# Optimization experiments

Measured on AMD Instinct MI355X. Metric: run time of the kernel, lower is better.

Reference implementation:

```python
import jax, jax.numpy as jnp
import numpy as np

B, S, D = 2, 2048, 2048
H, KV, HD = 32, 8, 64  # num_heads, num_key_value_heads, head_dim
ROPE_BASE = 10000.0


def setup_inputs() -> dict:
    key = jax.random.key(0)
    k1, k2, k3 = jax.random.split(key, 3)
    x = jax.random.normal(k1, (B, S, D), dtype=jnp.float32)
    # torch Linear weights are [out_features, in_features]
    w_qkv = jax.random.normal(k2, (H * HD + 2 * KV * HD, D), dtype=jnp.float32) * (D ** -0.5)
    w_out = jax.random.normal(k3, (D, D), dtype=jnp.float32) * (D ** -0.5)
    # true RoPE tables: cos/sin are [S, HD] with the half-frequencies duplicated
    inv_freq = 1.0 / (ROPE_BASE ** (jnp.arange(0, HD, 2, dtype=jnp.float32) / HD))
    angles = jnp.arange(S, dtype=jnp.float32)[:, None] * inv_freq[None, :]  # [S, HD/2]
    emb = jnp.concatenate([angles, angles], axis=-1)  # [S, HD]
    return {"x": x, "cos": jnp.cos(emb), "sin": jnp.sin(emb), "w_qkv": w_qkv, "w_out": w_out}


def _apply_rope(t, cos, sin):
    # t: [B, h, S, HD]; cos/sin: [S, HD]
    half = t.shape[-1] // 2
    t1, t2 = t[..., :half], t[..., half:]
    rot = jnp.concatenate([-t2, t1], axis=-1)
    return t * cos[None, None, :, :] + rot * sin[None, None, :, :]


def reference(x, cos, sin, w_qkv, w_out):
    b, s, d = x.shape
    qkv = jnp.einsum('bsd,od->bso', x, w_qkv)  # merged QKV projection
    q, k, v = jnp.split(qkv, [H * HD, H * HD + KV * HD], axis=-1)
    q = q.reshape(b, s, H, HD).transpose(0, 2, 1, 3)   # [b,H,s,hd]
    k = k.reshape(b, s, KV, HD).transpose(0, 2, 1, 3)  # [b,KV,s,hd]
    v = v.reshape(b, s, KV, HD).transpose(0, 2, 1, 3)
    q = _apply_rope(q, cos, sin)
    k = _apply_rope(k, cos, sin)
    n_rep = H // KV
    k = jnp.repeat(k, n_rep, axis=1)  # repeat_kv -> [b,H,s,hd]
    v = jnp.repeat(v, n_rep, axis=1)
    scale = HD ** -0.5
    scores = jnp.einsum('bhqd,bhkd->bhqk', q, k) * scale
    causal = jnp.tril(jnp.ones((s, s), dtype=bool))
    scores = jnp.where(causal[None, None], scores, jnp.finfo(scores.dtype).min)
    attn = jax.nn.softmax(scores, axis=-1)
    out = jnp.einsum('bhqk,bhkd->bhqd', attn, v)
    out = out.transpose(0, 2, 1, 3).reshape(b, s, H * HD)
    return jnp.einsum('bso,do->bsd', out, w_out)
```

## Files before the change

### kernel.cpp

```cpp
#include <hip/hip_runtime.h>
#include <hip/hip_fp16.h>

#define B_ 2
#define S_ 2048
#define D_ 2048
#define H_ 32
#define KV_ 8
#define HD_ 64

typedef unsigned short bf16_t;
typedef __attribute__((ext_vector_type(8))) short short8;
typedef __attribute__((ext_vector_type(4))) float floatx4;
typedef __attribute__((ext_vector_type(2))) float float2v;

__device__ __forceinline__ bf16_t f2bf(float f) {
  union { float f; unsigned u; } c; c.f = f;
  unsigned u = c.u;
  u += 0x7fffu + ((u >> 16) & 1u);
  return (bf16_t)(u >> 16);
}

__device__ __forceinline__ unsigned pk_bf16(float a, float b) {
#if __has_builtin(__builtin_amdgcn_cvt_pk_bf16_f32)
  auto v = __builtin_amdgcn_cvt_pk_bf16_f32(a, b);
  unsigned u; __builtin_memcpy(&u, &v, 4); return u;
#else
  return (unsigned)f2bf(a) | ((unsigned)f2bf(b) << 16);
#endif
}

__device__ __forceinline__ float fexp2(float x) {
#if __has_builtin(__builtin_amdgcn_exp2f)
  return __builtin_amdgcn_exp2f(x);
#else
  return exp2f(x);
#endif
}

__device__ __forceinline__ void load_lds16(const void* g, void* l) {
  __builtin_amdgcn_global_load_lds(
      (const __attribute__((address_space(1))) void*)g,
      (__attribute__((address_space(3))) void*)l, 16, 0, 0);
}

__device__ __forceinline__ void cvt4(const float* __restrict__ in,
                                     bf16_t* __restrict__ out, int i) {
  float4 v = ((const float4*)in)[i];
  ushort4 o;
  o.x = f2bf(v.x); o.y = f2bf(v.y); o.z = f2bf(v.z); o.w = f2bf(v.w);
  ((ushort4*)out)[i] = o;
}

__global__ __launch_bounds__(256) void prep(
    const float* __restrict__ x, bf16_t* __restrict__ xb,
    const float* __restrict__ wqkv, bf16_t* __restrict__ wqkvb,
    const float* __restrict__ wout, bf16_t* __restrict__ woutb,
    const float* __restrict__ cs, const float* __restrict__ sn,
    unsigned* __restrict__ tab) {
  const int bid = blockIdx.x;
  if (bid < 8192) {
    cvt4(x, xb, bid * 256 + threadIdx.x);
  } else if (bid < 14336) {
    cvt4(wqkv, wqkvb, (bid - 8192) * 256 + threadIdx.x);
  } else if (bid < 18432) {
    cvt4(wout, woutb, (bid - 14336) * 256 + threadIdx.x);
  } else {
    const int i = (bid - 18432) * 256 + threadIdx.x;
    __half2 h = __floats2half2_rn(cs[i], sn[i]);
    unsigned u; __builtin_memcpy(&u, &h, 4);
    tab[i] = u;
  }
}

__global__ __launch_bounds__(256) void gemm_bt(
    const bf16_t* __restrict__ A, const bf16_t* __restrict__ Bm,
    float* __restrict__ C, int M, int N, int K) {
  __shared__ __attribute__((aligned(16))) bf16_t As[128 * 32];
  __shared__ __attribute__((aligned(16))) bf16_t Bs[128 * 32];
  const int tid = threadIdx.x;
  const int lane = tid & 63;
  const int wave = tid >> 6;
  const int bm = blockIdx.y * 128, bn = blockIdx.x * 128;
  const int wm = (wave >> 1) * 64, wn = (wave & 1) * 64;
  const int lr = lane & 15, quad = lane >> 4;

  floatx4 acc[4][4] = {};

  const int t0 = tid, t1 = tid + 256;
  const int r0 = t0 >> 2, c0 = (t0 & 3) * 8;
  const int r1 = t1 >> 2, c1 = (t1 & 3) * 8;

  const bf16_t* Ab = A + (size_t)bm * K;
  const bf16_t* Bb = Bm + (size_t)bn * K;

  for (int k0 = 0; k0 < K; k0 += 32) {
    __syncthreads();
    load_lds16(Ab + (size_t)r0 * K + k0 + c0, &As[t0 * 8]);
    load_lds16(Ab + (size_t)r1 * K + k0 + c1, &As[t1 * 8]);
    load_lds16(Bb + (size_t)r0 * K + k0 + c0, &Bs[t0 * 8]);
    load_lds16(Bb + (size_t)r1 * K + k0 + c1, &Bs[t1 * 8]);
    __syncthreads();

    short8 af[4], bfr[4];
#pragma unroll
    for (int i = 0; i < 4; i++) {
      af[i]  = *(const short8*)&As[(wm + i * 16 + lr) * 32 + quad * 8];
      bfr[i] = *(const short8*)&Bs[(wn + i * 16 + lr) * 32 + quad * 8];
    }
#pragma unroll
    for (int mi = 0; mi < 4; mi++)
#pragma unroll
      for (int ni = 0; ni < 4; ni++)
        acc[mi][ni] = __builtin_amdgcn_mfma_f32_16x16x32_bf16(af[mi], bfr[ni], acc[mi][ni], 0, 0, 0);
  }

#pragma unroll
  for (int mi = 0; mi < 4; mi++) {
    const int row = bm + wm + mi * 16 + quad * 4;
#pragma unroll
    for (int ni = 0; ni < 4; ni++) {
      const int col = bn + wn + ni * 16 + lr;
      float* cp = C + (size_t)row * N + col;
#pragma unroll
      for (int r = 0; r < 4; r++) cp[(size_t)r * N] = acc[mi][ni][r];
    }
  }
}

__global__ __launch_bounds__(256, 4) void gemm_qkv(
    const bf16_t* __restrict__ A, const bf16_t* __restrict__ Bm,
    const unsigned* __restrict__ tab,
    bf16_t* __restrict__ q, bf16_t* __restrict__ k, bf16_t* __restrict__ vt) {
  const int K = 2048;
  __shared__ __attribute__((aligned(16))) bf16_t As[128 * 32];
  __shared__ __attribute__((aligned(16))) bf16_t Bs[128 * 32];
  __shared__ __attribute__((aligned(16))) bf16_t Ts[4][32 * 72];
  const int tid = threadIdx.x;
  const int lane = tid & 63;
  const int wave = tid >> 6;
  const int bm = blockIdx.y * 128, bn = blockIdx.x * 128;
  const int wm = (wave >> 1) * 64, wn = (wave & 1) * 64;
  const int lr = lane & 15, quad = lane >> 4;

  floatx4 acc[4][4] = {};

  const int t0 = tid, t1 = tid + 256;
  const int r0 = t0 >> 2, c0 = (t0 & 3) * 8;
  const int r1 = t1 >> 2, c1 = (t1 & 3) * 8;

  const bf16_t* Ab = A + (size_t)bm * K;
  const bf16_t* Bb = Bm + (size_t)bn * K;

  for (int k0 = 0; k0 < K; k0 += 32) {
    __syncthreads();
    load_lds16(Ab + (size_t)r0 * K + k0 + c0, &As[t0 * 8]);
    load_lds16(Ab + (size_t)r1 * K + k0 + c1, &As[t1 * 8]);
    load_lds16(Bb + (size_t)r0 * K + k0 + c0, &Bs[t0 * 8]);
    load_lds16(Bb + (size_t)r1 * K + k0 + c1, &Bs[t1 * 8]);
    __syncthreads();

    short8 af[4], bfr[4];
#pragma unroll
    for (int i = 0; i < 4; i++) {
      af[i]  = *(const short8*)&As[(wm + i * 16 + lr) * 32 + quad * 8];
      bfr[i] = *(const short8*)&Bs[(wn + i * 16 + lr) * 32 + quad * 8];
    }
#pragma unroll
    for (int mi = 0; mi < 4; mi++)
#pragma unroll
      for (int ni = 0; ni < 4; ni++)
        acc[mi][ni] = __builtin_amdgcn_mfma_f32_16x16x32_bf16(af[mi], bfr[ni], acc[mi][ni], 0, 0, 0);
  }

  const int f0 = bn + wn;
  const int srow0 = bm + wm;
  const int bb = srow0 >> 11, s0 = srow0 & 2047;

  if (f0 < 2560) {
    const bool isq = (f0 < 2048);
    const float scale = isq ? 0.18033688011f : 1.0f;
    bf16_t* dst = isq ? (q + (size_t)(bb * H_ + (f0 >> 6)) * S_ * HD_)
                      : (k + (size_t)(bb * KV_ + ((f0 - 2048) >> 6)) * S_ * HD_);
#pragma unroll
    for (int mi = 0; mi < 4; mi++) {
#pragma unroll
      for (int r = 0; r < 4; r++) {
        const int sr = s0 + mi * 16 + quad * 4 + r;
        const unsigned* tp = tab + (size_t)sr * HD_;
        bf16_t* drow = dst + (size_t)sr * HD_;
#pragma unroll
        for (int ni = 0; ni < 4; ni++) {
          const int d = ni * 16 + lr;
          const unsigned w = tp[d];
          __half2 h2; __builtin_memcpy(&h2, &w, 4);
          const float2 cf = __half22float2(h2);
          const float t = acc[mi][ni][r];
          const float oth = acc[mi][ni ^ 2][r];
          const float rot = (ni < 2) ? -oth : oth;
          drow[d] = f2bf((t * cf.x + rot * cf.y) * scale);
        }
      }
    }
  } else {
    const int hv = (f0 - 2560) >> 6;
    bf16_t* ts = Ts[wave];
    const int rl = lane >> 1, hf = lane & 1;
#pragma unroll
    for (int p = 0; p < 2; p++) {
#pragma unroll
      for (int nn = 0; nn < 2; nn++) {
        const int ni = 2 * p + nn;
#pragma unroll
        for (int mi = 0; mi < 4; mi++) {
          uint2 pw;
          pw.x = pk_bf16(acc[mi][ni][0], acc[mi][ni][1]);
          pw.y = pk_bf16(acc[mi][ni][2], acc[mi][ni][3]);
          *(uint2*)&ts[(nn * 16 + lr) * 72 + mi * 16 + quad * 4] = pw;
        }
      }
      bf16_t* vrow = vt + ((size_t)(bb * KV_ + hv) * HD_ + p * 32 + rl) * S_ + s0 + hf * 32;
#pragma unroll
      for (int j = 0; j < 4; j++)
        *(short8*)(vrow + j * 8) = *(const short8*)&ts[rl * 72 + hf * 32 + j * 8];
    }
  }
}

__device__ __forceinline__ void stage64(const bf16_t* __restrict__ gbase, int rstride,
                                        bf16_t* lbuf, int wave, int lane) {
  const int sub = lane >> 3;
  const int sc  = lane & 7;
  const int gc  = sc ^ sub;
#pragma unroll
  for (int j = 0; j < 2; j++) {
    const int r = wave * 16 + j * 8 + sub;
    load_lds16(gbase + (size_t)r * rstride + gc * 8,
               lbuf + (wave * 128 + j * 64 + lane) * 8);
  }
}

__device__ __forceinline__ void softmax_ps(
    floatx4* st, bool diag, int qg, int kk, float& m, float& l,
    floatx4* o, bf16_t* pl, int lr, int quad, int sw) {
  if (diag) {
#pragma unroll
    for (int t = 0; t < 4; t++)
#pragma unroll
      for (int r = 0; r < 4; r++) {
        const int kg = kk + t * 16 + quad * 4 + r;
        st[t][r] = (kg <= qg) ? st[t][r] : -1e30f;
      }
  }
  float mx = -3e30f;
#pragma unroll
  for (int t = 0; t < 4; t++)
#pragma unroll
    for (int r = 0; r < 4; r++) mx = fmaxf(mx, st[t][r]);
  mx = fmaxf(mx, __shfl_xor(mx, 16, 64));
  mx = fmaxf(mx, __shfl_xor(mx, 32, 64));
  const float mn = fmaxf(m, mx);
  float rs = 0.f;
#pragma unroll
  for (int t = 0; t < 4; t++)
#pragma unroll
    for (int r = 0; r < 4; r++) {
      const float p = fexp2(st[t][r] - mn);
      st[t][r] = p;
      rs += p;
    }
  rs += __shfl_xor(rs, 16, 64);
  rs += __shfl_xor(rs, 32, 64);
  if (__all(mn == m)) {
    l += rs;
  } else {
    const float a = fexp2(m - mn);
    l = l * a + rs;
    m = mn;
    const floatx4 a4 = { a, a, a, a };
#pragma unroll
    for (int dt = 0; dt < 4; dt++) o[dt] *= a4;
  }
#pragma unroll
  for (int t = 0; t < 4; t++) {
    uint2 pw;
    pw.x = pk_bf16(st[t][0], st[t][1]);
    pw.y = pk_bf16(st[t][2], st[t][3]);
    *(uint2*)&pl[lr * 64 + (((2 * t + (quad >> 1)) ^ sw) * 8) + (quad & 1) * 4] = pw;
  }
}

__device__ __forceinline__ void store_o(
    const floatx4* o, float l, bf16_t* __restrict__ O,
    int b, int h, int q0, int lr, int quad) {
  const float linv = 1.f / l;
  const floatx4 lv = { linv, linv, linv, linv };
  bf16_t* ob = O + ((size_t)b * S_ + q0 + lr) * (H_ * HD_) + h * HD_ + quad * 4;
#pragma unroll
  for (int dt = 0; dt < 4; dt++) {
    const floatx4 ov = o[dt] * lv;
    uint2 pw;
    pw.x = pk_bf16(ov[0], ov[1]);
    pw.y = pk_bf16(ov[2], ov[3]);
    *(uint2*)(ob + dt * 16) = pw;
  }
}

__device__ __forceinline__ void attn_half(
    const bf16_t* __restrict__ Q, const bf16_t* __restrict__ kb,
    const bf16_t* __restrict__ vb, bf16_t* __restrict__ O,
    bf16_t* Ks, bf16_t* Vs, bf16_t* pla, bf16_t* plb,
    int bh, int T, int wave, int lr, int quad) {
  const int b = bh >> 5, h = bh & 31;
  const int lane = quad * 16 + lr;
  const int sw = lr & 7;
  const int qa0 = T * 128 + wave * 16;
  const int qb0 = qa0 + 64;
  const bf16_t* qpa = Q + ((size_t)bh * S_ + qa0) * HD_;
  const short8 qfa0 = *(const short8*)(qpa + lr * HD_ + quad * 8);
  const short8 qfa1 = *(const short8*)(qpa + lr * HD_ + 32 + quad * 8);
  const short8 qfb0 = *(const short8*)(qpa + (64 + lr) * HD_ + quad * 8);
  const short8 qfb1 = *(const short8*)(qpa + (64 + lr) * HD_ + 32 + quad * 8);

  floatx4 oa[4] = {}, ob[4] = {};
  float ma = -1e30f, la = 0.f, mb = -1e30f, lb = 0.f;
  const int qga = qa0 + lr, qgb = qb0 + lr;
  const int nt = 2 * T + 2;

  stage64(kb, HD_, Ks, wave, lane);
  stage64(vb, S_, Vs, wave, lane);

  for (int kt = 0; kt < nt; kt++) {
    const int kk = kt * 64;
    bf16_t* Kc = Ks + (kt & 1) * 4096;
    bf16_t* Vc = Vs + (kt & 1) * 4096;
    __syncthreads();
    if (kt + 1 < nt) {
      stage64(kb + (size_t)(kk + 64) * HD_, HD_, Ks + ((kt + 1) & 1) * 4096, wave, lane);
      stage64(vb + (kk + 64), S_, Vs + ((kt + 1) & 1) * 4096, wave, lane);
    }
    const bool doA  = (kt <= 2 * T);
    const bool dgA  = (kt == 2 * T);
    const bool dgB  = (kt == nt - 1);

    floatx4 sta[4] = {}, stb[4] = {};
#pragma unroll
    for (int t = 0; t < 4; t++) {
      const int R = t * 16 + lr;
      const short8 kf0 = *(const short8*)&Kc[R * 64 + ((quad ^ sw) * 8)];
      const short8 kf1 = *(const short8*)&Kc[R * 64 + (((4 + quad) ^ sw) * 8)];
      if (doA) {
        sta[t] = __builtin_amdgcn_mfma_f32_16x16x32_bf16(kf0, qfa0, sta[t], 0, 0, 0);
        sta[t] = __builtin_amdgcn_mfma_f32_16x16x32_bf16(kf1, qfa1, sta[t], 0, 0, 0);
      }
      stb[t] = __builtin_amdgcn_mfma_f32_16x16x32_bf16(kf0, qfb0, stb[t], 0, 0, 0);
      stb[t] = __builtin_amdgcn_mfma_f32_16x16x32_bf16(kf1, qfb1, stb[t], 0, 0, 0);
    }
    if (doA) softmax_ps(sta, dgA, qga, kk, ma, la, oa, pla, lr, quad, sw);
    softmax_ps(stb, dgB, qgb, kk, mb, lb, ob, plb, lr, quad, sw);

    short8 pfa0, pfa1;
    if (doA) {
      pfa0 = *(const short8*)&pla[lr * 64 + ((quad ^ sw) * 8)];
      pfa1 = *(const short8*)&pla[lr * 64 + (((4 + quad) ^ sw) * 8)];
    }
    const short8 pfb0 = *(const short8*)&plb[lr * 64 + ((quad ^ sw) * 8)];
    const short8 pfb1 = *(const short8*)&plb[lr * 64 + (((4 + quad) ^ sw) * 8)];
#pragma unroll
    for (int dt = 0; dt < 4; dt++) {
      const int Rv = dt * 16 + lr;
      const short8 vf0 = *(const short8*)&Vc[Rv * 64 + ((quad ^ sw) * 8)];
      const short8 vf1 = *(const short8*)&Vc[Rv * 64 + (((4 + quad) ^ sw) * 8)];
      if (doA) {
        oa[dt] = __builtin_amdgcn_mfma_f32_16x16x32_bf16(vf0, pfa0, oa[dt], 0, 0, 0);
        oa[dt] = __builtin_amdgcn_mfma_f32_16x16x32_bf16(vf1, pfa1, oa[dt], 0, 0, 0);
      }
      ob[dt] = __builtin_amdgcn_mfma_f32_16x16x32_bf16(vf0, pfb0, ob[dt], 0, 0, 0);
      ob[dt] = __builtin_amdgcn_mfma_f32_16x16x32_bf16(vf1, pfb1, ob[dt], 0, 0, 0);
    }
  }

  store_o(oa, la, O, b, h, qa0, lr, quad);
  store_o(ob, lb, O, b, h, qb0, lr, quad);
}

__global__ __launch_bounds__(256, 2) void flash_attn(
    const bf16_t* __restrict__ Q,
    const bf16_t* __restrict__ Kc,
    const bf16_t* __restrict__ Vt,
    bf16_t* __restrict__ O) {
  __shared__ __attribute__((aligned(16))) bf16_t Ks[2 * 4096];
  __shared__ __attribute__((aligned(16))) bf16_t Vs[2 * 4096];
  __shared__ __attribute__((aligned(16))) bf16_t Pl[8192];
  const int bh = blockIdx.y;
  const int b = bh >> 5, h = bh & 31;
  const int kvh = b * KV_ + (h >> 2);
  const int wave = threadIdx.x >> 6, lane = threadIdx.x & 63;
  const int lr = lane & 15, quad = lane >> 4;

  const bf16_t* kb = Kc + (size_t)kvh * S_ * HD_;
  const bf16_t* vb = Vt + (size_t)kvh * HD_ * S_;
  bf16_t* pla = Pl + wave * 2048;
  bf16_t* plb = pla + 1024;

  const int ta = blockIdx.x;
  const int tb = 15 - blockIdx.x;
  attn_half(Q, kb, vb, O, Ks, Vs, pla, plb, bh, ta, wave, lr, quad);
  __syncthreads();
  attn_half(Q, kb, vb, O, Ks, Vs, pla, plb, bh, tb, wave, lr, quad);
}

extern "C" void kernel_launch(void* const* d_in, const int* in_sizes, int n_in,
                              void* d_out, int out_size, void* d_ws, size_t ws_size,
                              hipStream_t stream) {
  const float* x    = (const float*)d_in[0];
  const float* cs   = (const float*)d_in[1];
  const float* sn   = (const float*)d_in[2];
  const float* wqkv = (const float*)d_in[3];
  const float* wout = (const float*)d_in[4];
  float* out = (float*)d_out;

  char* ws = (char*)d_ws;
  bf16_t*  xb    = (bf16_t*)(ws);
  bf16_t*  wqkvb = (bf16_t*)(ws + 16777216);
  bf16_t*  woutb = (bf16_t*)(ws + 29360128);
  bf16_t*  qb    = (bf16_t*)(ws + 37748736);
  bf16_t*  kb    = (bf16_t*)(ws + 54525952);
  bf16_t*  vtb   = (bf16_t*)(ws + 58720256);
  bf16_t*  attnb = (bf16_t*)(ws + 62914560);
  unsigned* tab  = (unsigned*)(ws + 79691776);

  prep<<<18944, 256, 0, stream>>>(x, xb, wqkv, wqkvb, wout, woutb, cs, sn, tab);
  gemm_qkv<<<dim3(24, 32), 256, 0, stream>>>(xb, wqkvb, tab, qb, kb, vtb);
  flash_attn<<<dim3(8, 64), 256, 0, stream>>>(qb, kb, vtb, attnb);
  gemm_bt<<<dim3(16, 32), 256, 0, stream>>>(attnb, woutb, out, 4096, 2048, 2048);
}
```

Before: 313.6 us.

## Rewrite flash attention with 32x32 MFMA and register-resident P fragments

The flash attention kernel moves from 16x16x32 MFMA tiles over 4 waves to 32x32x16 MFMA tiles over 2 waves, each wave owning 32 query rows. P is now rebuilt into B-operand fragments in registers through a permlane32 swap instead of a round trip through LDS, which removes the Pl shared buffer. It also adds a lazy max rescale that only rescales when the new max exceeds the old by more than 8, plus s_setprio around the MFMA blocks. The grid becomes 16x64 blocks of 128 threads, each handling a paired 64-row causal tile, which changes occupancy and load balance.

```diff
diff --git a/kernel.cpp b/kernel.cpp
--- a/kernel.cpp
+++ b/kernel.cpp
@@ -11,7 +11,7 @@
 typedef unsigned short bf16_t;
 typedef __attribute__((ext_vector_type(8))) short short8;
 typedef __attribute__((ext_vector_type(4))) float floatx4;
-typedef __attribute__((ext_vector_type(2))) float float2v;
+typedef __attribute__((ext_vector_type(16))) float floatx16;
 
 __device__ __forceinline__ bf16_t f2bf(float f) {
   union { float f; unsigned u; } c; c.f = f;
@@ -226,187 +226,191 @@
   }
 }
 
-__device__ __forceinline__ void stage64(const bf16_t* __restrict__ gbase, int rstride,
-                                        bf16_t* lbuf, int wave, int lane) {
+
+__device__ __forceinline__ void stage64x2(const bf16_t* __restrict__ g, int rstride,
+                                          bf16_t* lbuf, int wave, int lane) {
   const int sub = lane >> 3;
   const int sc  = lane & 7;
   const int gc  = sc ^ sub;
 #pragma unroll
-  for (int j = 0; j < 2; j++) {
-    const int r = wave * 16 + j * 8 + sub;
-    load_lds16(gbase + (size_t)r * rstride + gc * 8,
-               lbuf + (wave * 128 + j * 64 + lane) * 8);
-  }
-}
-
-__device__ __forceinline__ void softmax_ps(
-    floatx4* st, bool diag, int qg, int kk, float& m, float& l,
-    floatx4* o, bf16_t* pl, int lr, int quad, int sw) {
-  if (diag) {
-#pragma unroll
-    for (int t = 0; t < 4; t++)
-#pragma unroll
-      for (int r = 0; r < 4; r++) {
-        const int kg = kk + t * 16 + quad * 4 + r;
-        st[t][r] = (kg <= qg) ? st[t][r] : -1e30f;
-      }
-  }
-  float mx = -3e30f;
-#pragma unroll
-  for (int t = 0; t < 4; t++)
-#pragma unroll
-    for (int r = 0; r < 4; r++) mx = fmaxf(mx, st[t][r]);
-  mx = fmaxf(mx, __shfl_xor(mx, 16, 64));
-  mx = fmaxf(mx, __shfl_xor(mx, 32, 64));
-  const float mn = fmaxf(m, mx);
-  float rs = 0.f;
-#pragma unroll
-  for (int t = 0; t < 4; t++)
-#pragma unroll
-    for (int r = 0; r < 4; r++) {
-      const float p = fexp2(st[t][r] - mn);
-      st[t][r] = p;
-      rs += p;
-    }
-  rs += __shfl_xor(rs, 16, 64);
-  rs += __shfl_xor(rs, 32, 64);
-  if (__all(mn == m)) {
-    l += rs;
-  } else {
-    const float a = fexp2(m - mn);
-    l = l * a + rs;
-    m = mn;
-    const floatx4 a4 = { a, a, a, a };
-#pragma unroll
-    for (int dt = 0; dt < 4; dt++) o[dt] *= a4;
-  }
-#pragma unroll
-  for (int t = 0; t < 4; t++) {
-    uint2 pw;
-    pw.x = pk_bf16(st[t][0], st[t][1]);
-    pw.y = pk_bf16(st[t][2], st[t][3]);
-    *(uint2*)&pl[lr * 64 + (((2 * t + (quad >> 1)) ^ sw) * 8) + (quad & 1) * 4] = pw;
-  }
-}
-
-__device__ __forceinline__ void store_o(
-    const floatx4* o, float l, bf16_t* __restrict__ O,
-    int b, int h, int q0, int lr, int quad) {
-  const float linv = 1.f / l;
-  const floatx4 lv = { linv, linv, linv, linv };
-  bf16_t* ob = O + ((size_t)b * S_ + q0 + lr) * (H_ * HD_) + h * HD_ + quad * 4;
-#pragma unroll
-  for (int dt = 0; dt < 4; dt++) {
-    const floatx4 ov = o[dt] * lv;
-    uint2 pw;
-    pw.x = pk_bf16(ov[0], ov[1]);
-    pw.y = pk_bf16(ov[2], ov[3]);
-    *(uint2*)(ob + dt * 16) = pw;
-  }
-}
-
-__device__ __forceinline__ void attn_half(
+  for (int j = 0; j < 4; j++) {
+    const int r = wave * 32 + j * 8 + sub;
+    load_lds16(g + (size_t)r * rstride + gc * 8,
+               lbuf + (wave * 256 + j * 64 + lane) * 8);
+  }
+}
+
+__device__ __forceinline__ void hswap(unsigned a, unsigned b, unsigned& x, unsigned& y) {
+#if __has_builtin(__builtin_amdgcn_permlane32_swap)
+  auto r = __builtin_amdgcn_permlane32_swap(a, b, false, false);
+  x = (unsigned)r[0]; y = (unsigned)r[1];
+#else
+  const unsigned pa = (unsigned)__shfl_xor((int)a, 32, 64);
+  const unsigned pb = (unsigned)__shfl_xor((int)b, 32, 64);
+  const bool hi = (threadIdx.x & 32) != 0;
+  x = hi ? pb : a;
+  y = hi ? b : pa;
+#endif
+}
+
+__device__ __forceinline__ void build_pfrag(const floatx16& p, short8& f0, short8& f1) {
+  unsigned w[8];
+  const unsigned c01 = pk_bf16(p[0], p[1]);
+  const unsigned c45 = pk_bf16(p[4], p[5]);
+  const unsigned c23 = pk_bf16(p[2], p[3]);
+  const unsigned c67 = pk_bf16(p[6], p[7]);
+  hswap(c01, c45, w[0], w[2]);
+  hswap(c23, c67, w[1], w[3]);
+  const unsigned d01 = pk_bf16(p[8], p[9]);
+  const unsigned d45 = pk_bf16(p[12], p[13]);
+  const unsigned d23 = pk_bf16(p[10], p[11]);
+  const unsigned d67 = pk_bf16(p[14], p[15]);
+  hswap(d01, d45, w[4], w[6]);
+  hswap(d23, d67, w[5], w[7]);
+  __builtin_memcpy(&f0, &w[0], 16);
+  __builtin_memcpy(&f1, &w[4], 16);
+}
+
+__device__ __forceinline__ void attn_half32(
     const bf16_t* __restrict__ Q, const bf16_t* __restrict__ kb,
     const bf16_t* __restrict__ vb, bf16_t* __restrict__ O,
-    bf16_t* Ks, bf16_t* Vs, bf16_t* pla, bf16_t* plb,
-    int bh, int T, int wave, int lr, int quad) {
-  const int b = bh >> 5, h = bh & 31;
-  const int lane = quad * 16 + lr;
-  const int sw = lr & 7;
-  const int qa0 = T * 128 + wave * 16;
-  const int qb0 = qa0 + 64;
-  const bf16_t* qpa = Q + ((size_t)bh * S_ + qa0) * HD_;
-  const short8 qfa0 = *(const short8*)(qpa + lr * HD_ + quad * 8);
-  const short8 qfa1 = *(const short8*)(qpa + lr * HD_ + 32 + quad * 8);
-  const short8 qfb0 = *(const short8*)(qpa + (64 + lr) * HD_ + quad * 8);
-  const short8 qfb1 = *(const short8*)(qpa + (64 + lr) * HD_ + 32 + quad * 8);
-
-  floatx4 oa[4] = {}, ob[4] = {};
-  float ma = -1e30f, la = 0.f, mb = -1e30f, lb = 0.f;
-  const int qga = qa0 + lr, qgb = qb0 + lr;
-  const int nt = 2 * T + 2;
-
-  stage64(kb, HD_, Ks, wave, lane);
-  stage64(vb, S_, Vs, wave, lane);
+    bf16_t* Ks, bf16_t* Vs, int b, int h, int bh, int T, int wave, int lane) {
+  const int nt = T + 1;
+  const int q0 = T * 64 + wave * 32;
+  const int cq = lane & 31;
+  const int hh = lane >> 5;
+  const int sw7 = lane & 7;
+
+  const bf16_t* qp = Q + ((size_t)bh * S_ + q0 + cq) * HD_ + hh * 8;
+  short8 qf[4];
+#pragma unroll
+  for (int ds = 0; ds < 4; ds++) qf[ds] = *(const short8*)(qp + ds * 16);
+
+  floatx16 o0 = {}, o1 = {};
+  float m = -1e30f, l = 0.f;
+
+  stage64x2(kb, HD_, Ks, wave, lane);
+  stage64x2(vb, S_, Vs, wave, lane);
 
   for (int kt = 0; kt < nt; kt++) {
-    const int kk = kt * 64;
-    bf16_t* Kc = Ks + (kt & 1) * 4096;
-    bf16_t* Vc = Vs + (kt & 1) * 4096;
     __syncthreads();
     if (kt + 1 < nt) {
-      stage64(kb + (size_t)(kk + 64) * HD_, HD_, Ks + ((kt + 1) & 1) * 4096, wave, lane);
-      stage64(vb + (kk + 64), S_, Vs + ((kt + 1) & 1) * 4096, wave, lane);
-    }
-    const bool doA  = (kt <= 2 * T);
-    const bool dgA  = (kt == 2 * T);
-    const bool dgB  = (kt == nt - 1);
-
-    floatx4 sta[4] = {}, stb[4] = {};
-#pragma unroll
-    for (int t = 0; t < 4; t++) {
-      const int R = t * 16 + lr;
-      const short8 kf0 = *(const short8*)&Kc[R * 64 + ((quad ^ sw) * 8)];
-      const short8 kf1 = *(const short8*)&Kc[R * 64 + (((4 + quad) ^ sw) * 8)];
-      if (doA) {
-        sta[t] = __builtin_amdgcn_mfma_f32_16x16x32_bf16(kf0, qfa0, sta[t], 0, 0, 0);
-        sta[t] = __builtin_amdgcn_mfma_f32_16x16x32_bf16(kf1, qfa1, sta[t], 0, 0, 0);
+      stage64x2(kb + (size_t)(kt + 1) * 64 * HD_, HD_, Ks + ((kt + 1) & 1) * 4096, wave, lane);
+      stage64x2(vb + (kt + 1) * 64, S_, Vs + ((kt + 1) & 1) * 4096, wave, lane);
+    }
+    const bf16_t* Kc = Ks + (kt & 1) * 4096;
+    const bf16_t* Vc = Vs + (kt & 1) * 4096;
+
+    floatx16 s0 = {}, s1 = {};
+    __builtin_amdgcn_s_setprio(1);
+#pragma unroll
+    for (int ds = 0; ds < 4; ds++) {
+      const int slot = (((ds * 2 + hh) ^ sw7) * 8);
+      const short8 k0 = *(const short8*)&Kc[cq * 64 + slot];
+      const short8 k1 = *(const short8*)&Kc[(32 + cq) * 64 + slot];
+      s0 = __builtin_amdgcn_mfma_f32_32x32x16_bf16(k0, qf[ds], s0, 0, 0, 0);
+      s1 = __builtin_amdgcn_mfma_f32_32x32x16_bf16(k1, qf[ds], s1, 0, 0, 0);
+    }
+    __builtin_amdgcn_s_setprio(0);
+
+    if (kt == T) {
+      const int qg = q0 + cq;
+      const int kbase = kt * 64 + 4 * hh;
+#pragma unroll
+      for (int r = 0; r < 16; r++) {
+        const int kg = kbase + (r & 3) + 8 * (r >> 2);
+        s0[r] = (kg <= qg) ? s0[r] : -1e30f;
+        s1[r] = (kg + 32 <= qg) ? s1[r] : -1e30f;
       }
-      stb[t] = __builtin_amdgcn_mfma_f32_16x16x32_bf16(kf0, qfb0, stb[t], 0, 0, 0);
-      stb[t] = __builtin_amdgcn_mfma_f32_16x16x32_bf16(kf1, qfb1, stb[t], 0, 0, 0);
-    }
-    if (doA) softmax_ps(sta, dgA, qga, kk, ma, la, oa, pla, lr, quad, sw);
-    softmax_ps(stb, dgB, qgb, kk, mb, lb, ob, plb, lr, quad, sw);
-
-    short8 pfa0, pfa1;
-    if (doA) {
-      pfa0 = *(const short8*)&pla[lr * 64 + ((quad ^ sw) * 8)];
-      pfa1 = *(const short8*)&pla[lr * 64 + (((4 + quad) ^ sw) * 8)];
-    }
-    const short8 pfb0 = *(const short8*)&plb[lr * 64 + ((quad ^ sw) * 8)];
-    const short8 pfb1 = *(const short8*)&plb[lr * 64 + (((4 + quad) ^ sw) * 8)];
-#pragma unroll
-    for (int dt = 0; dt < 4; dt++) {
-      const int Rv = dt * 16 + lr;
-      const short8 vf0 = *(const short8*)&Vc[Rv * 64 + ((quad ^ sw) * 8)];
-      const short8 vf1 = *(const short8*)&Vc[Rv * 64 + (((4 + quad) ^ sw) * 8)];
-      if (doA) {
-        oa[dt] = __builtin_amdgcn_mfma_f32_16x16x32_bf16(vf0, pfa0, oa[dt], 0, 0, 0);
-        oa[dt] = __builtin_amdgcn_mfma_f32_16x16x32_bf16(vf1, pfa1, oa[dt], 0, 0, 0);
-      }
-      ob[dt] = __builtin_amdgcn_mfma_f32_16x16x32_bf16(vf0, pfb0, ob[dt], 0, 0, 0);
-      ob[dt] = __builtin_amdgcn_mfma_f32_16x16x32_bf16(vf1, pfb1, ob[dt], 0, 0, 0);
-    }
-  }
-
-  store_o(oa, la, O, b, h, qa0, lr, quad);
-  store_o(ob, lb, O, b, h, qb0, lr, quad);
-}
-
-__global__ __launch_bounds__(256, 2) void flash_attn(
+    }
+
+    float t[8];
+#pragma unroll
+    for (int i = 0; i < 8; i++)
+      t[i] = fmaxf(fmaxf(s0[i], s0[i + 8]), fmaxf(s1[i], s1[i + 8]));
+#pragma unroll
+    for (int st = 4; st >= 1; st >>= 1)
+#pragma unroll
+      for (int i = 0; i < st; i++) t[i] = fmaxf(t[i], t[i + st]);
+    float mx = t[0];
+    mx = fmaxf(mx, __shfl_xor(mx, 32, 64));
+
+    if (!__all(mx <= m + 8.0f)) {
+      const float mn = fmaxf(m, mx);
+      const float a = fexp2(m - mn);
+      l *= a;
+#pragma unroll
+      for (int i = 0; i < 16; i++) { o0[i] *= a; o1[i] *= a; }
+      m = mn;
+    }
+
+#pragma unroll
+    for (int i = 0; i < 16; i++) {
+      s0[i] = fexp2(s0[i] - m);
+      s1[i] = fexp2(s1[i] - m);
+    }
+    float u[8];
+#pragma unroll
+    for (int i = 0; i < 8; i++)
+      u[i] = (s0[i] + s0[i + 8]) + (s1[i] + s1[i + 8]);
+#pragma unroll
+    for (int st = 4; st >= 1; st >>= 1)
+#pragma unroll
+      for (int i = 0; i < st; i++) u[i] += u[i + st];
+    l += u[0];
+
+    short8 pf[4];
+    build_pfrag(s0, pf[0], pf[1]);
+    build_pfrag(s1, pf[2], pf[3]);
+
+    __builtin_amdgcn_s_setprio(1);
+#pragma unroll
+    for (int ks = 0; ks < 4; ks++) {
+      const int slot = (((ks * 2 + hh) ^ sw7) * 8);
+      const short8 v0 = *(const short8*)&Vc[cq * 64 + slot];
+      const short8 v1 = *(const short8*)&Vc[(32 + cq) * 64 + slot];
+      o0 = __builtin_amdgcn_mfma_f32_32x32x16_bf16(v0, pf[ks], o0, 0, 0, 0);
+      o1 = __builtin_amdgcn_mfma_f32_32x32x16_bf16(v1, pf[ks], o1, 0, 0, 0);
+    }
+    __builtin_amdgcn_s_setprio(0);
+  }
+
+  const float lt = l + __shfl_xor(l, 32, 64);
+  const float li = 1.f / lt;
+  bf16_t* ob = O + ((size_t)b * S_ + q0 + cq) * (H_ * HD_) + h * HD_ + hh * 4;
+#pragma unroll
+  for (int rq = 0; rq < 4; rq++) {
+    uint2 w0;
+    w0.x = pk_bf16(o0[4 * rq] * li, o0[4 * rq + 1] * li);
+    w0.y = pk_bf16(o0[4 * rq + 2] * li, o0[4 * rq + 3] * li);
+    *(uint2*)(ob + rq * 8) = w0;
+    uint2 w1;
+    w1.x = pk_bf16(o1[4 * rq] * li, o1[4 * rq + 1] * li);
+    w1.y = pk_bf16(o1[4 * rq + 2] * li, o1[4 * rq + 3] * li);
+    *(uint2*)(ob + 32 + rq * 8) = w1;
+  }
+}
+
+__global__ __launch_bounds__(128, 2) void flash_attn(
     const bf16_t* __restrict__ Q,
     const bf16_t* __restrict__ Kc,
     const bf16_t* __restrict__ Vt,
     bf16_t* __restrict__ O) {
   __shared__ __attribute__((aligned(16))) bf16_t Ks[2 * 4096];
   __shared__ __attribute__((aligned(16))) bf16_t Vs[2 * 4096];
-  __shared__ __attribute__((aligned(16))) bf16_t Pl[8192];
   const int bh = blockIdx.y;
   const int b = bh >> 5, h = bh & 31;
   const int kvh = b * KV_ + (h >> 2);
   const int wave = threadIdx.x >> 6, lane = threadIdx.x & 63;
-  const int lr = lane & 15, quad = lane >> 4;
 
   const bf16_t* kb = Kc + (size_t)kvh * S_ * HD_;
   const bf16_t* vb = Vt + (size_t)kvh * HD_ * S_;
-  bf16_t* pla = Pl + wave * 2048;
-  bf16_t* plb = pla + 1024;
 
   const int ta = blockIdx.x;
-  const int tb = 15 - blockIdx.x;
-  attn_half(Q, kb, vb, O, Ks, Vs, pla, plb, bh, ta, wave, lr, quad);
+  const int tb = 31 - blockIdx.x;
+  attn_half32(Q, kb, vb, O, Ks, Vs, b, h, bh, ta, wave, lane);
   __syncthreads();
-  attn_half(Q, kb, vb, O, Ks, Vs, pla, plb, bh, tb, wave, lr, quad);
+  attn_half32(Q, kb, vb, O, Ks, Vs, b, h, bh, tb, wave, lane);
 }
 
 extern "C" void kernel_launch(void* const* d_in, const int* in_sizes, int n_in,
@@ -431,6 +435,6 @@
 
   prep<<<18944, 256, 0, stream>>>(x, xb, wqkv, wqkvb, wout, woutb, cs, sn, tab);
   gemm_qkv<<<dim3(24, 32), 256, 0, stream>>>(xb, wqkvb, tab, qb, kb, vtb);
-  flash_attn<<<dim3(8, 64), 256, 0, stream>>>(qb, kb, vtb, attnb);
+  flash_attn<<<dim3(16, 64), 128, 0, stream>>>(qb, kb, vtb, attnb);
   gemm_bt<<<dim3(16, 32), 256, 0, stream>>>(attnb, woutb, out, 4096, 2048, 2048);
 }
```

After: 305.7 us. -2.5%, faster.
